# Optimization experiments

Hardware: AMD Instinct MI355X
Metric: run time of the kernel (lower is better)

Reference implementation:

```python
import jax, jax.numpy as jnp
import numpy as np
import math

B, H, S, D = 2, 8, 1024, 384
LAMBDA_INIT = 0.8 - 0.6 * math.exp(-0.3 * 1)  # depth = 1


def _clin(xr, xi, wr, wi, br=None, bi=None):
    # complex linear: (xr + i xi) @ (wr + i wi)^T + (br + i bi)
    o_r = jnp.einsum('bhse,de->bhsd', xr, wr) - jnp.einsum('bhse,de->bhsd', xi, wi)
    o_i = jnp.einsum('bhse,de->bhsd', xr, wi) + jnp.einsum('bhse,de->bhsd', xi, wr)
    if br is not None:
        o_r = o_r + br
        o_i = o_i + bi
    return o_r, o_i


def _attn_w(qr, qi, kr, ki, scale):
    # complex score magnitude -> softmax
    s_r = jnp.einsum('bhqd,bhkd->bhqk', qr, kr) + jnp.einsum('bhqd,bhkd->bhqk', qi, ki)
    s_i = jnp.einsum('bhqd,bhkd->bhqk', qi, kr) - jnp.einsum('bhqd,bhkd->bhqk', qr, ki)
    return jax.nn.softmax(jnp.sqrt(s_r ** 2 + s_i ** 2 + 1e-8) * scale, axis=-1)


def setup_inputs() -> dict:
    key = jax.random.key(0)
    ks = jax.random.split(key, 32)
    n = lambda k, sh, std=1.0: jax.random.normal(k, sh, dtype=jnp.float32) * std
    sd = 1.0 / math.sqrt(D)
    inp = {
        'q_r': n(ks[0], (B, H, S, D)), 'q_i': n(ks[1], (B, H, S, D)),
        'k_r': n(ks[2], (B, H, S, D)), 'k_i': n(ks[3], (B, H, S, D)),
        'v_r': n(ks[4], (B, H, S, D)), 'v_i': n(ks[5], (B, H, S, D)),
        'pe_q_r': n(ks[6], (B, H, S, D)), 'pe_q_i': n(ks[7], (B, H, S, D)),
        'pe_k_r': n(ks[8], (B, H, S, D)), 'pe_k_i': n(ks[9], (B, H, S, D)),
        'wq_r': n(ks[10], (2 * D, D), sd), 'wq_i': n(ks[11], (2 * D, D), sd),
        'bq_r': jnp.zeros((2 * D,), jnp.float32), 'bq_i': jnp.zeros((2 * D,), jnp.float32),
        'wk_r': n(ks[12], (D, D), sd), 'wk_i': n(ks[13], (D, D), sd),
        'bk_r': jnp.zeros((D,), jnp.float32), 'bk_i': jnp.zeros((D,), jnp.float32),
        'wv_r': n(ks[14], (D, D), sd), 'wv_i': n(ks[15], (D, D), sd),
        'bv_r': jnp.zeros((D,), jnp.float32), 'bv_i': jnp.zeros((D,), jnp.float32),
        'wg_r': n(ks[16], (D, D), sd), 'wg_i': n(ks[17], (D, D), sd),
        'bg_r': jnp.zeros((D,), jnp.float32), 'bg_i': jnp.zeros((D,), jnp.float32),
        'wo_r': n(ks[18], (D, D), sd), 'wo_i': n(ks[19], (D, D), sd),
        'bo_r': jnp.zeros((D,), jnp.float32), 'bo_i': jnp.zeros((D,), jnp.float32),
        'lam_q1': n(ks[20], (D,), 0.1), 'lam_k1': n(ks[21], (D,), 0.1),
        'lam_q2': n(ks[22], (D,), 0.1), 'lam_k2': n(ks[23], (D,), 0.1),
        'subln_w': jnp.ones((2 * D,), jnp.float32),
    }
    return inp


def reference(q_r, q_i, k_r, k_i, v_r, v_i, pe_q_r, pe_q_i, pe_k_r, pe_k_i,
              wq_r, wq_i, bq_r, bq_i, wk_r, wk_i, bk_r, bk_i,
              wv_r, wv_i, bv_r, bv_i, wg_r, wg_i, bg_r, bg_i,
              wo_r, wo_i, bo_r, bo_i, lam_q1, lam_k1, lam_q2, lam_k2, subln_w):
    scale = D ** (-0.5)
    qp_r, qp_i = _clin(q_r, q_i, wq_r, wq_i, bq_r, bq_i)   # [B,H,S,2D]
    kp_r, kp_i = _clin(k_r, k_i, wk_r, wk_i, bk_r, bk_i)   # [B,H,S,D]
    vp_r, vp_i = _clin(v_r, v_i, wv_r, wv_i, bv_r, bv_i)
    qp_r = qp_r + jnp.concatenate([pe_q_r, pe_q_r], axis=-1)
    qp_i = qp_i + jnp.concatenate([pe_q_i, pe_q_i], axis=-1)
    kp_r = kp_r + pe_k_r
    kp_i = kp_i + pe_k_i
    q1_r, q2_r = jnp.split(qp_r, 2, axis=-1)
    q1_i, q2_i = jnp.split(qp_i, 2, axis=-1)
    w1 = _attn_w(q1_r, q1_i, kp_r, kp_i, scale)
    w2 = _attn_w(q2_r, q2_i, kp_r, kp_i, scale)
    a1_r = jnp.einsum('bhqk,bhkd->bhqd', w1, vp_r)
    a1_i = jnp.einsum('bhqk,bhkd->bhqd', w1, vp_i)
    a2_r = jnp.einsum('bhqk,bhkd->bhqd', w2, vp_r)
    a2_i = jnp.einsum('bhqk,bhkd->bhqd', w2, vp_i)
    cat_r = jnp.concatenate([a1_r, a2_r], axis=-1)
    cat_i = jnp.concatenate([a1_i, a2_i], axis=-1)
    # complex RMSNorm (SubLN) over 2D dim
    rms = jnp.sqrt(jnp.mean(cat_r ** 2 + cat_i ** 2, axis=-1, keepdims=True) + 1e-5)
    cat_r = cat_r / rms * subln_w
    cat_i = cat_i / rms * subln_w
    a1_r, a2_r = jnp.split(cat_r, 2, axis=-1)
    a1_i, a2_i = jnp.split(cat_i, 2, axis=-1)
    lam1 = jnp.exp(jnp.sum(lam_q1 * lam_k1))
    lam2 = jnp.exp(jnp.sum(lam_q2 * lam_k2))
    lam = jax.nn.sigmoid(lam1 - lam2 + LAMBDA_INIT)
    out_r = a1_r - lam * a2_r
    out_i = a1_i - lam * a2_i
    g_r, g_i = _clin(q_r, q_i, wg_r, wg_i, bg_r, bg_i)
    out_r, out_i = g_r * out_r - g_i * out_i, g_r * out_i + g_i * out_r
    out_r, out_i = _clin(out_r, out_i, wo_r, wo_i, bo_r, bo_i)
    return (out_r, out_i)
```

## Files before the change

kernel.cpp:

```cpp
#include <hip/hip_runtime.h>
#include <cstdint>


typedef _Float16 f16;
typedef __attribute__((ext_vector_type(8))) _Float16 f16x8;
typedef __attribute__((ext_vector_type(4))) _Float16 f16x4;
typedef __attribute__((ext_vector_type(4))) float    f32x4;

#define NROW      16384L
#define HALF_OUT  6291456L
#define SCALE_QK  0.05103103630798288f
#define LAMBDA_INIT 0.35550906759096926f

__device__ __forceinline__ void gl2lds16(const void* g, void* l) {
  __builtin_amdgcn_global_load_lds(
      (const __attribute__((address_space(1))) void*)(uintptr_t)g,
      (__attribute__((address_space(3))) void*)(uint32_t)(uintptr_t)l,
      16, 0, 0);
}

struct PeTab { const float* p[6]; float sgn[6]; };

enum { MODE_PROJ = 0, MODE_VT = 1, MODE_OUT = 2 };

template <int MODE>
__launch_bounds__(256, 2)
__global__ void gemm_kernel(const f16* __restrict__ A, int lda,
                            const f16* __restrict__ W, int ldw,
                            const float* __restrict__ bias, PeTab pe,
                            void* __restrict__ outp, int ldo, int K, int gx)
{
  __shared__ f16 As[2][128 * 32];
  __shared__ f16 Bs[2][128 * 32];
  const int t    = threadIdx.x;
  const int lane = t & 63;
  const int wave = t >> 6;
  const int bid  = blockIdx.x;
  const int xcd  = bid & 7;
  const int per  = bid >> 3;
  const long row0 = (long)(xcd * 16 + per / gx) * 128;
  const long col0 = (long)(per % gx) * 128;
  const f16* Ab = A + row0 * (long)lda;
  const f16* Wb = W + col0 * (long)ldw;

  const int wm = (wave >> 1) * 64;
  const int wn = (wave & 1) * 64;
  const int lm = lane & 15;
  const int lk = (lane >> 4) * 8;

  f32x4 acc[4][4] = {};

  auto stage = [&](int kk, int sub) {
#pragma unroll
    for (int j = 0; j < 2; ++j) {
      int sg = j * 256 + t, r = sg >> 2, c = (sg & 3) << 3;
      gl2lds16(Ab + (long)r * lda + kk + c, &As[sub][sg * 8]);
      gl2lds16(Wb + (long)r * ldw + kk + c, &Bs[sub][sg * 8]);
    }
  };

  for (int kk = 0; kk < K; kk += 64) {
    stage(kk, 0);
    stage(kk + 32, 1);
    __syncthreads();
#pragma unroll
    for (int sub = 0; sub < 2; ++sub) {
      f16x8 bfr[4];
#pragma unroll
      for (int nt = 0; nt < 4; ++nt)
        bfr[nt] = *(const f16x8*)&Bs[sub][(wn + nt * 16 + lm) * 32 + lk];
#pragma unroll
      for (int mt = 0; mt < 4; ++mt) {
        f16x8 afr = *(const f16x8*)&As[sub][(wm + mt * 16 + lm) * 32 + lk];
#pragma unroll
        for (int nt = 0; nt < 4; ++nt)
          acc[mt][nt] = __builtin_amdgcn_mfma_f32_16x16x32_f16(afr, bfr[nt], acc[mt][nt], 0, 0, 0);
      }
    }
    __syncthreads();
  }

  const int lm4 = (lane >> 4) * 4;
  const int ln  = lane & 15;
#pragma unroll
  for (int mt = 0; mt < 4; ++mt) {
#pragma unroll
    for (int nt = 0; nt < 4; ++nt) {
      int col = (int)col0 + wn + nt * 16 + ln;
      if (MODE == MODE_VT) {
        long rowb = row0 + wm + mt * 16 + lm4;
        long bh = rowb >> 10, sx = rowb & 1023;
        f16x4 v;
#pragma unroll
        for (int r = 0; r < 4; ++r) v[r] = (f16)(acc[mt][nt][r] + bias[col]);
        *(f16x4*)&((f16*)outp)[(bh * 768 + col) * 1024 + sx] = v;
      } else {
#pragma unroll
        for (int r = 0; r < 4; ++r) {
          long row = row0 + wm + mt * 16 + lm4 + r;
          float c = acc[mt][nt][r] + bias[col];
          if (MODE == MODE_PROJ) {
            int s2 = col / 384;
            int d  = col - s2 * 384;
            const float* pp = pe.p[s2];
            if (pp) c += pe.sgn[s2] * pp[row * 384 + d];
            ((f16*)outp)[row * (long)ldo + col] = (f16)c;
          } else {
            float* of = (float*)outp;
            if (col < 384) of[row * 384 + col] = c;
            else           of[HALF_OUT + row * 384 + (col - 384)] = c;
          }
        }
      }
    }
  }
}

__launch_bounds__(256, 2)
__global__ void score_kernel(const f16* __restrict__ QG, const f16* __restrict__ Kc,
                             f16* __restrict__ P)
{
  __shared__ f16 AsL[128 * 32], AsH[128 * 32], BsL[128 * 32], BsH[128 * 32];
  const int t = threadIdx.x, lane = t & 63, wave = t >> 6;
  const int bid = blockIdx.x;
  const int xcd = bid & 7, per = bid >> 3;
  const int z   = xcd * 4 + per / 64;
  const int rem = per % 64;
  const int w = z >> 4, bh = z & 15;
  const long row0 = (long)(rem / 8) * 128, col0 = (long)(rem % 8) * 128;
  const f16* A = QG + (long)bh * 1024 * 2304 + row0 * 2304 + w * 768;
  const f16* B = Kc + (long)bh * 1024 * 768 + col0 * 768;
  f16* Pz = P + (long)z * 1024 * 1024;

  const int wm = (wave >> 1) * 64, wn = (wave & 1) * 64;
  const int lm = lane & 15, lk = (lane >> 4) * 8;
  f32x4 accr[4][4] = {}, acci[4][4] = {};

  for (int kk = 0; kk < 384; kk += 32) {
#pragma unroll
    for (int j = 0; j < 2; ++j) {
      int sg = j * 256 + t, r = sg >> 2, c = (sg & 3) << 3;
      gl2lds16(A + (long)r * 2304 + kk + c,       &AsL[sg * 8]);
      gl2lds16(A + (long)r * 2304 + 384 + kk + c, &AsH[sg * 8]);
      gl2lds16(B + (long)r * 768 + kk + c,        &BsL[sg * 8]);
      gl2lds16(B + (long)r * 768 + 384 + kk + c,  &BsH[sg * 8]);
    }
    __syncthreads();
    f16x8 bl[4], bh2[4];
#pragma unroll
    for (int nt = 0; nt < 4; ++nt) {
      bl[nt]  = *(const f16x8*)&BsL[(wn + nt * 16 + lm) * 32 + lk];
      bh2[nt] = *(const f16x8*)&BsH[(wn + nt * 16 + lm) * 32 + lk];
    }
#pragma unroll
    for (int mt = 0; mt < 4; ++mt) {
      f16x8 al  = *(const f16x8*)&AsL[(wm + mt * 16 + lm) * 32 + lk];
      f16x8 ah  = *(const f16x8*)&AsH[(wm + mt * 16 + lm) * 32 + lk];
      f16x8 nal = -al;
#pragma unroll
      for (int nt = 0; nt < 4; ++nt) {
        accr[mt][nt] = __builtin_amdgcn_mfma_f32_16x16x32_f16(al,  bl[nt],  accr[mt][nt], 0, 0, 0);
        accr[mt][nt] = __builtin_amdgcn_mfma_f32_16x16x32_f16(ah,  bh2[nt], accr[mt][nt], 0, 0, 0);
        acci[mt][nt] = __builtin_amdgcn_mfma_f32_16x16x32_f16(ah,  bl[nt],  acci[mt][nt], 0, 0, 0);
        acci[mt][nt] = __builtin_amdgcn_mfma_f32_16x16x32_f16(nal, bh2[nt], acci[mt][nt], 0, 0, 0);
      }
    }
    __syncthreads();
  }
  const int lm4 = (lane >> 4) * 4, ln = lane & 15;
#pragma unroll
  for (int mt = 0; mt < 4; ++mt)
#pragma unroll
    for (int nt = 0; nt < 4; ++nt) {
      int col = (int)col0 + wn + nt * 16 + ln;
#pragma unroll
      for (int r = 0; r < 4; ++r) {
        long row = row0 + wm + mt * 16 + lm4 + r;
        float sr = accr[mt][nt][r], si = acci[mt][nt][r];
        float m = sqrtf(sr * sr + si * si + 1e-8f) * SCALE_QK;
        Pz[row * 1024 + col] = (f16)m;
      }
    }
}

__launch_bounds__(256, 2)
__global__ void pv_kernel(const f16* __restrict__ P, const f16* __restrict__ Vt,
                          f16* __restrict__ O1, f16* __restrict__ O2)
{
  __shared__ f16 As1[2][128 * 32], As2[2][128 * 32], Bs[2][128 * 32];
  const int t = threadIdx.x, lane = t & 63, wave = t >> 6;
  const int bid = blockIdx.x;
  const int xcd = bid & 7, per = bid >> 3;
  const int bh  = xcd * 2 + per / 48;
  const int rem = per % 48;
  const long row0 = (long)(rem / 6) * 128, col0 = (long)(rem % 6) * 128;
  const f16* A1 = P + ((long)bh << 20) + row0 * 1024;
  const f16* A2 = P + ((long)(16 + bh) << 20) + row0 * 1024;
  const f16* B  = Vt + (long)bh * 768 * 1024 + col0 * 1024;

  const int wm = (wave >> 1) * 64, wn = (wave & 1) * 64;
  const int lm = lane & 15, lk = (lane >> 4) * 8;
  f32x4 ac1[4][4] = {}, ac2[4][4] = {};

  auto stage = [&](int kk, int sub) {
#pragma unroll
    for (int j = 0; j < 2; ++j) {
      int sg = j * 256 + t, r = sg >> 2, c = (sg & 3) << 3;
      gl2lds16(A1 + (long)r * 1024 + kk + c, &As1[sub][sg * 8]);
      gl2lds16(A2 + (long)r * 1024 + kk + c, &As2[sub][sg * 8]);
      gl2lds16(B  + (long)r * 1024 + kk + c, &Bs[sub][sg * 8]);
    }
  };

  for (int kk = 0; kk < 1024; kk += 64) {
    stage(kk, 0);
    stage(kk + 32, 1);
    __syncthreads();
#pragma unroll
    for (int sub = 0; sub < 2; ++sub) {
      f16x8 bfr[4];
#pragma unroll
      for (int nt = 0; nt < 4; ++nt)
        bfr[nt] = *(const f16x8*)&Bs[sub][(wn + nt * 16 + lm) * 32 + lk];
#pragma unroll
      for (int mt = 0; mt < 4; ++mt) {
        f16x8 a1 = *(const f16x8*)&As1[sub][(wm + mt * 16 + lm) * 32 + lk];
        f16x8 a2 = *(const f16x8*)&As2[sub][(wm + mt * 16 + lm) * 32 + lk];
#pragma unroll
        for (int nt = 0; nt < 4; ++nt) {
          ac1[mt][nt] = __builtin_amdgcn_mfma_f32_16x16x32_f16(a1, bfr[nt], ac1[mt][nt], 0, 0, 0);
          ac2[mt][nt] = __builtin_amdgcn_mfma_f32_16x16x32_f16(a2, bfr[nt], ac2[mt][nt], 0, 0, 0);
        }
      }
    }
    __syncthreads();
  }
  const int lm4 = (lane >> 4) * 4, ln = lane & 15;
#pragma unroll
  for (int mt = 0; mt < 4; ++mt)
#pragma unroll
    for (int nt = 0; nt < 4; ++nt) {
      int col = (int)col0 + wn + nt * 16 + ln;
#pragma unroll
      for (int r = 0; r < 4; ++r) {
        long row = (long)bh * 1024 + row0 + wm + mt * 16 + lm4 + r;
        O1[row * 768 + col] = (f16)ac1[mt][nt][r];
        O2[row * 768 + col] = (f16)ac2[mt][nt][r];
      }
    }
}

__global__ void softmax_kernel(f16* __restrict__ P)
{
  const long row = blockIdx.x;
  f16* p = P + row * 1024;
  const int lane = threadIdx.x;
  f16x8 v0 = *(const f16x8*)(p + lane * 16);
  f16x8 v1 = *(const f16x8*)(p + lane * 16 + 8);
  float x[16];
#pragma unroll
  for (int i = 0; i < 8; ++i) { x[i] = (float)v0[i]; x[8 + i] = (float)v1[i]; }
  float m = x[0];
#pragma unroll
  for (int i = 1; i < 16; ++i) m = fmaxf(m, x[i]);
#pragma unroll
  for (int off = 1; off < 64; off <<= 1) m = fmaxf(m, __shfl_xor(m, off));
  float s = 0.f;
#pragma unroll
  for (int i = 0; i < 16; ++i) { x[i] = __expf(x[i] - m); s += x[i]; }
#pragma unroll
  for (int off = 1; off < 64; off <<= 1) s += __shfl_xor(s, off);
  float inv = 1.f / s;
  f16x8 o0, o1;
#pragma unroll
  for (int i = 0; i < 8; ++i) { o0[i] = (f16)(x[i] * inv); o1[i] = (f16)(x[8 + i] * inv); }
  *(f16x8*)(p + lane * 16)     = o0;
  *(f16x8*)(p + lane * 16 + 8) = o1;
}

__global__ void fuse_kernel(const f16* __restrict__ A1, const f16* __restrict__ A2,
                            const f16* __restrict__ QG, const float* __restrict__ subw,
                            const float* __restrict__ lamp, f16* __restrict__ Xatt)
{
  const long row = blockIdx.x;
  const int t = threadIdx.x, lane = t & 63, wv = t >> 6;
  const f16* a1 = A1 + row * 768;
  const f16* a2 = A2 + row * 768;
  const f16* g  = QG + row * 2304 + 1536;
  float a1r[3], a1i[3], a2r[3], a2i[3];
  float ss = 0.f;
#pragma unroll
  for (int q = 0; q < 3; ++q) {
    int d = t + q * 128;
    a1r[q] = (float)a1[d]; a1i[q] = (float)a1[d + 384];
    a2r[q] = (float)a2[d]; a2i[q] = (float)a2[d + 384];
    ss += a1r[q] * a1r[q] + a1i[q] * a1i[q] + a2r[q] * a2r[q] + a2i[q] * a2i[q];
  }
#pragma unroll
  for (int m = 1; m < 64; m <<= 1) ss += __shfl_xor(ss, m);
  __shared__ float part[2];
  if (lane == 0) part[wv] = ss;
  __syncthreads();
  float inv = rsqrtf((part[0] + part[1]) * (1.f / 768.f) + 1e-5f);
  float lam = lamp[0];
#pragma unroll
  for (int q = 0; q < 3; ++q) {
    int d = t + q * 128;
    float w1 = subw[d], w2 = subw[d + 384];
    float n1r = a1r[q] * inv * w1, n1i = a1i[q] * inv * w1;
    float n2r = a2r[q] * inv * w2, n2i = a2i[q] * inv * w2;
    float orr = n1r - lam * n2r, oii = n1i - lam * n2i;
    float gr = (float)g[d], gi = (float)g[d + 384];
    Xatt[row * 768 + d]       = (f16)(gr * orr - gi * oii);
    Xatt[row * 768 + d + 384] = (f16)(gr * oii + gi * orr);
  }
}

__global__ void lam_kernel(const float* lq1, const float* lk1,
                           const float* lq2, const float* lk2, float* out)
{
  const int t = threadIdx.x, lane = t & 63, wv = t >> 6;
  float s1 = 0.f, s2 = 0.f;
#pragma unroll
  for (int q = 0; q < 3; ++q) {
    int d = t + q * 128;
    s1 += lq1[d] * lk1[d];
    s2 += lq2[d] * lk2[d];
  }
#pragma unroll
  for (int m = 1; m < 64; m <<= 1) { s1 += __shfl_xor(s1, m); s2 += __shfl_xor(s2, m); }
  __shared__ float p1[2], p2[2];
  if (lane == 0) { p1[wv] = s1; p2[wv] = s2; }
  __syncthreads();
  if (t == 0) {
    float x = expf(p1[0] + p1[1]) - expf(p2[0] + p2[1]) + LAMBDA_INIT;
    out[0] = 1.f / (1.f + expf(-x));
  }
}

__global__ void pack_x(const float* __restrict__ xr, const float* __restrict__ xi,
                       f16* __restrict__ X)
{
  long i = (long)blockIdx.x * 256 + threadIdx.x;
  long row = i / 768;
  int  c   = (int)(i - row * 768);
  float v = (c < 384) ? xr[row * 384 + c] : xi[row * 384 + (c - 384)];
  X[i] = (f16)v;
}

__global__ void pack_wq(const float* wq_r, const float* wq_i,
                        const float* wg_r, const float* wg_i,
                        const float* bq_r, const float* bq_i,
                        const float* bg_r, const float* bg_i,
                        f16* __restrict__ Wp, float* __restrict__ bp)
{
  long i = (long)blockIdx.x * 256 + threadIdx.x;
  int n = (int)(i / 768), e = (int)(i % 768);
  int s = n / 384, d = n - s * 384;
  int hb = (e >= 384);
  int ee = e - hb * 384;
  float v = 0.f, b = 0.f;
  switch (s) {
    case 0: v = hb ? -wq_i[d * 384 + ee]         :  wq_r[d * 384 + ee];         b = bq_r[d];       break;
    case 1: v = hb ?  wq_r[d * 384 + ee]         :  wq_i[d * 384 + ee];         b = bq_i[d];       break;
    case 2: v = hb ? -wq_i[(384 + d) * 384 + ee] :  wq_r[(384 + d) * 384 + ee]; b = bq_r[384 + d]; break;
    case 3: v = hb ?  wq_r[(384 + d) * 384 + ee] :  wq_i[(384 + d) * 384 + ee]; b = bq_i[384 + d]; break;
    case 4: v = hb ? -wg_i[d * 384 + ee]         :  wg_r[d * 384 + ee];         b = bg_r[d];       break;
    case 5: v = hb ?  wg_r[d * 384 + ee]         :  wg_i[d * 384 + ee];         b = bg_i[d];       break;
  }
  Wp[i] = (f16)v;
  if (e == 0) bp[n] = b;
}

__global__ void pack_w_std(const float* wr, const float* wi,
                           const float* br, const float* bi,
                           f16* __restrict__ Wp, float* __restrict__ bp)
{
  long i = (long)blockIdx.x * 256 + threadIdx.x;
  int n = (int)(i / 768), e = (int)(i % 768);
  int hb = (e >= 384);
  int ee = e - hb * 384;
  float v, b;
  if (n < 384) { v = hb ? -wi[n * 384 + ee] : wr[n * 384 + ee]; b = br[n]; }
  else { int d = n - 384; v = hb ? wr[d * 384 + ee] : wi[d * 384 + ee]; b = bi[d]; }
  Wp[i] = (f16)v;
  if (e == 0) bp[n] = b;
}

extern "C" void kernel_launch(void* const* d_in, const int* in_sizes, int n_in,
                              void* d_out, int out_size, void* d_ws, size_t ws_size,
                              hipStream_t stream)
{
  const float* q_r    = (const float*)d_in[0];
  const float* q_i    = (const float*)d_in[1];
  const float* k_r    = (const float*)d_in[2];
  const float* k_i    = (const float*)d_in[3];
  const float* v_r    = (const float*)d_in[4];
  const float* v_i    = (const float*)d_in[5];
  const float* pe_q_r = (const float*)d_in[6];
  const float* pe_q_i = (const float*)d_in[7];
  const float* pe_k_r = (const float*)d_in[8];
  const float* pe_k_i = (const float*)d_in[9];
  const float* wq_r = (const float*)d_in[10];
  const float* wq_i = (const float*)d_in[11];
  const float* bq_r = (const float*)d_in[12];
  const float* bq_i = (const float*)d_in[13];
  const float* wk_r = (const float*)d_in[14];
  const float* wk_i = (const float*)d_in[15];
  const float* bk_r = (const float*)d_in[16];
  const float* bk_i = (const float*)d_in[17];
  const float* wv_r = (const float*)d_in[18];
  const float* wv_i = (const float*)d_in[19];
  const float* bv_r = (const float*)d_in[20];
  const float* bv_i = (const float*)d_in[21];
  const float* wg_r = (const float*)d_in[22];
  const float* wg_i = (const float*)d_in[23];
  const float* bg_r = (const float*)d_in[24];
  const float* bg_i = (const float*)d_in[25];
  const float* wo_r = (const float*)d_in[26];
  const float* wo_i = (const float*)d_in[27];
  const float* bo_r = (const float*)d_in[28];
  const float* bo_i = (const float*)d_in[29];
  const float* lam_q1 = (const float*)d_in[30];
  const float* lam_k1 = (const float*)d_in[31];
  const float* lam_q2 = (const float*)d_in[32];
  const float* lam_k2 = (const float*)d_in[33];
  const float* subln_w = (const float*)d_in[34];

  char* base = (char*)d_ws;
  size_t off = 0;
  auto alloc = [&](size_t bytes) -> void* {
    void* p = base + off;
    off = (off + bytes + 255) & ~(size_t)255;
    return p;
  };
  f16*   Wq   = (f16*)alloc(2304L * 768 * 2);
  f16*   Wk   = (f16*)alloc(768L * 768 * 2);
  f16*   Wv   = (f16*)alloc(768L * 768 * 2);
  f16*   Wo   = (f16*)alloc(768L * 768 * 2);
  float* bq   = (float*)alloc(2304 * 4);
  float* bk   = (float*)alloc(768 * 4);
  float* bv   = (float*)alloc(768 * 4);
  float* bo   = (float*)alloc(768 * 4);
  float* lamp = (float*)alloc(4);
  f16*   X    = (f16*)alloc(NROW * 768 * 2);
  f16*   QG   = (f16*)alloc(NROW * 2304 * 2);
  f16*   Kc   = (f16*)alloc(NROW * 768 * 2);
  f16*   Vt   = (f16*)alloc(16L * 768 * 1024 * 2);
  f16*   P    = (f16*)alloc(32L * 1024 * 1024 * 2);
  if (off > ws_size) return;
  f16* A1   = Kc;
  f16* A2   = X;
  f16* Xatt = Vt;

  pack_wq<<<6912, 256, 0, stream>>>(wq_r, wq_i, wg_r, wg_i, bq_r, bq_i, bg_r, bg_i, Wq, bq);
  pack_w_std<<<2304, 256, 0, stream>>>(wk_r, wk_i, bk_r, bk_i, Wk, bk);
  pack_w_std<<<2304, 256, 0, stream>>>(wv_r, wv_i, bv_r, bv_i, Wv, bv);
  pack_w_std<<<2304, 256, 0, stream>>>(wo_r, wo_i, bo_r, bo_i, Wo, bo);
  lam_kernel<<<1, 128, 0, stream>>>(lam_q1, lam_k1, lam_q2, lam_k2, lamp);

  PeTab pe0{};

  pack_x<<<49152, 256, 0, stream>>>(q_r, q_i, X);
  PeTab peQ{};
  peQ.p[0] = pe_q_r; peQ.sgn[0] = 1.f;
  peQ.p[1] = pe_q_i; peQ.sgn[1] = 1.f;
  peQ.p[2] = pe_q_r; peQ.sgn[2] = 1.f;
  peQ.p[3] = pe_q_i; peQ.sgn[3] = 1.f;
  gemm_kernel<MODE_PROJ><<<2304, 256, 0, stream>>>(
      X, 768, Wq, 768, bq, peQ, QG, 2304, 768, 18);

  pack_x<<<49152, 256, 0, stream>>>(k_r, k_i, X);
  PeTab peK{};
  peK.p[0] = pe_k_r; peK.sgn[0] = 1.f;
  peK.p[1] = pe_k_i; peK.sgn[1] = 1.f;
  gemm_kernel<MODE_PROJ><<<768, 256, 0, stream>>>(
      X, 768, Wk, 768, bk, peK, Kc, 768, 768, 6);

  pack_x<<<49152, 256, 0, stream>>>(v_r, v_i, X);
  gemm_kernel<MODE_VT><<<768, 256, 0, stream>>>(
      X, 768, Wv, 768, bv, pe0, Vt, 0, 768, 6);

  score_kernel<<<2048, 256, 0, stream>>>(QG, Kc, P);
  softmax_kernel<<<32768, 64, 0, stream>>>(P);
  pv_kernel<<<768, 256, 0, stream>>>(P, Vt, A1, A2);

  fuse_kernel<<<16384, 128, 0, stream>>>(A1, A2, QG, subln_w, lamp, Xatt);

  gemm_kernel<MODE_OUT><<<768, 256, 0, stream>>>(
      Xatt, 768, Wo, 768, bo, pe0, d_out, 0, 768, 6);

  (void)in_sizes; (void)n_in; (void)out_size;
}
```

Before: 829.8 us.

## Double-buffer LDS staging in GEMMs and vectorize pack/softmax launches

The gemm, score and pv kernels now prefetch the next 32-wide K slice into an alternate LDS buffer while the current slice feeds the MFMAs. This is meant to hide global-load latency behind compute. The score kernel's LDS doubles to 64 KB, which may limit occupancy at two blocks per CU. pack_x now converts 8 elements per thread with a vector store, and softmax packs 4 rows per 256-thread block to cut launch and block overhead. There is only one barrier per iteration, placed after compute. That looks safe because the next prefetch goes to the buffer just read, which is fenced by that barrier, but it relies on the asynchronous LDS loads completing before the barrier.

```diff
diff --git a/kernel.cpp b/kernel.cpp
--- a/kernel.cpp
+++ b/kernel.cpp
@@ -59,25 +59,24 @@
     }
   };
 
-  for (int kk = 0; kk < K; kk += 64) {
-    stage(kk, 0);
-    stage(kk + 32, 1);
+  stage(0, 0);
+  __syncthreads();
+  int cur = 0;
+  for (int kk = 0; kk < K; kk += 32) {
+    if (kk + 32 < K) stage(kk + 32, cur ^ 1);
+    f16x8 bfr[4];
+#pragma unroll
+    for (int nt = 0; nt < 4; ++nt)
+      bfr[nt] = *(const f16x8*)&Bs[cur][(wn + nt * 16 + lm) * 32 + lk];
+#pragma unroll
+    for (int mt = 0; mt < 4; ++mt) {
+      f16x8 afr = *(const f16x8*)&As[cur][(wm + mt * 16 + lm) * 32 + lk];
+#pragma unroll
+      for (int nt = 0; nt < 4; ++nt)
+        acc[mt][nt] = __builtin_amdgcn_mfma_f32_16x16x32_f16(afr, bfr[nt], acc[mt][nt], 0, 0, 0);
+    }
     __syncthreads();
-#pragma unroll
-    for (int sub = 0; sub < 2; ++sub) {
-      f16x8 bfr[4];
-#pragma unroll
-      for (int nt = 0; nt < 4; ++nt)
-        bfr[nt] = *(const f16x8*)&Bs[sub][(wn + nt * 16 + lm) * 32 + lk];
-#pragma unroll
-      for (int mt = 0; mt < 4; ++mt) {
-        f16x8 afr = *(const f16x8*)&As[sub][(wm + mt * 16 + lm) * 32 + lk];
-#pragma unroll
-        for (int nt = 0; nt < 4; ++nt)
-          acc[mt][nt] = __builtin_amdgcn_mfma_f32_16x16x32_f16(afr, bfr[nt], acc[mt][nt], 0, 0, 0);
-      }
-    }
-    __syncthreads();
+    cur ^= 1;
   }
 
   const int lm4 = (lane >> 4) * 4;
@@ -120,7 +119,8 @@
 __global__ void score_kernel(const f16* __restrict__ QG, const f16* __restrict__ Kc,
                              f16* __restrict__ P)
 {
-  __shared__ f16 AsL[128 * 32], AsH[128 * 32], BsL[128 * 32], BsH[128 * 32];
+  __shared__ f16 AsL[2][128 * 32], AsH[2][128 * 32];
+  __shared__ f16 BsL[2][128 * 32], BsH[2][128 * 32];
   const int t = threadIdx.x, lane = t & 63, wave = t >> 6;
   const int bid = blockIdx.x;
   const int xcd = bid & 7, per = bid >> 3;
@@ -136,26 +136,32 @@
   const int lm = lane & 15, lk = (lane >> 4) * 8;
   f32x4 accr[4][4] = {}, acci[4][4] = {};
 
-  for (int kk = 0; kk < 384; kk += 32) {
+  auto stage = [&](int kk, int sub) {
 #pragma unroll
     for (int j = 0; j < 2; ++j) {
       int sg = j * 256 + t, r = sg >> 2, c = (sg & 3) << 3;
-      gl2lds16(A + (long)r * 2304 + kk + c,       &AsL[sg * 8]);
-      gl2lds16(A + (long)r * 2304 + 384 + kk + c, &AsH[sg * 8]);
-      gl2lds16(B + (long)r * 768 + kk + c,        &BsL[sg * 8]);
-      gl2lds16(B + (long)r * 768 + 384 + kk + c,  &BsH[sg * 8]);
-    }
-    __syncthreads();
+      gl2lds16(A + (long)r * 2304 + kk + c,       &AsL[sub][sg * 8]);
+      gl2lds16(A + (long)r * 2304 + 384 + kk + c, &AsH[sub][sg * 8]);
+      gl2lds16(B + (long)r * 768 + kk + c,        &BsL[sub][sg * 8]);
+      gl2lds16(B + (long)r * 768 + 384 + kk + c,  &BsH[sub][sg * 8]);
+    }
+  };
+
+  stage(0, 0);
+  __syncthreads();
+  int cur = 0;
+  for (int kk = 0; kk < 384; kk += 32) {
+    if (kk + 32 < 384) stage(kk + 32, cur ^ 1);
     f16x8 bl[4], bh2[4];
 #pragma unroll
     for (int nt = 0; nt < 4; ++nt) {
-      bl[nt]  = *(const f16x8*)&BsL[(wn + nt * 16 + lm) * 32 + lk];
-      bh2[nt] = *(const f16x8*)&BsH[(wn + nt * 16 + lm) * 32 + lk];
+      bl[nt]  = *(const f16x8*)&BsL[cur][(wn + nt * 16 + lm) * 32 + lk];
+      bh2[nt] = *(const f16x8*)&BsH[cur][(wn + nt * 16 + lm) * 32 + lk];
     }
 #pragma unroll
     for (int mt = 0; mt < 4; ++mt) {
-      f16x8 al  = *(const f16x8*)&AsL[(wm + mt * 16 + lm) * 32 + lk];
-      f16x8 ah  = *(const f16x8*)&AsH[(wm + mt * 16 + lm) * 32 + lk];
+      f16x8 al  = *(const f16x8*)&AsL[cur][(wm + mt * 16 + lm) * 32 + lk];
+      f16x8 ah  = *(const f16x8*)&AsH[cur][(wm + mt * 16 + lm) * 32 + lk];
       f16x8 nal = -al;
 #pragma unroll
       for (int nt = 0; nt < 4; ++nt) {
@@ -166,6 +172,7 @@
       }
     }
     __syncthreads();
+    cur ^= 1;
   }
   const int lm4 = (lane >> 4) * 4, ln = lane & 15;
 #pragma unroll
@@ -212,28 +219,27 @@
     }
   };
 
-  for (int kk = 0; kk < 1024; kk += 64) {
-    stage(kk, 0);
-    stage(kk + 32, 1);
+  stage(0, 0);
+  __syncthreads();
+  int cur = 0;
+  for (int kk = 0; kk < 1024; kk += 32) {
+    if (kk + 32 < 1024) stage(kk + 32, cur ^ 1);
+    f16x8 bfr[4];
+#pragma unroll
+    for (int nt = 0; nt < 4; ++nt)
+      bfr[nt] = *(const f16x8*)&Bs[cur][(wn + nt * 16 + lm) * 32 + lk];
+#pragma unroll
+    for (int mt = 0; mt < 4; ++mt) {
+      f16x8 a1 = *(const f16x8*)&As1[cur][(wm + mt * 16 + lm) * 32 + lk];
+      f16x8 a2 = *(const f16x8*)&As2[cur][(wm + mt * 16 + lm) * 32 + lk];
+#pragma unroll
+      for (int nt = 0; nt < 4; ++nt) {
+        ac1[mt][nt] = __builtin_amdgcn_mfma_f32_16x16x32_f16(a1, bfr[nt], ac1[mt][nt], 0, 0, 0);
+        ac2[mt][nt] = __builtin_amdgcn_mfma_f32_16x16x32_f16(a2, bfr[nt], ac2[mt][nt], 0, 0, 0);
+      }
+    }
     __syncthreads();
-#pragma unroll
-    for (int sub = 0; sub < 2; ++sub) {
-      f16x8 bfr[4];
-#pragma unroll
-      for (int nt = 0; nt < 4; ++nt)
-        bfr[nt] = *(const f16x8*)&Bs[sub][(wn + nt * 16 + lm) * 32 + lk];
-#pragma unroll
-      for (int mt = 0; mt < 4; ++mt) {
-        f16x8 a1 = *(const f16x8*)&As1[sub][(wm + mt * 16 + lm) * 32 + lk];
-        f16x8 a2 = *(const f16x8*)&As2[sub][(wm + mt * 16 + lm) * 32 + lk];
-#pragma unroll
-        for (int nt = 0; nt < 4; ++nt) {
-          ac1[mt][nt] = __builtin_amdgcn_mfma_f32_16x16x32_f16(a1, bfr[nt], ac1[mt][nt], 0, 0, 0);
-          ac2[mt][nt] = __builtin_amdgcn_mfma_f32_16x16x32_f16(a2, bfr[nt], ac2[mt][nt], 0, 0, 0);
-        }
-      }
-    }
-    __syncthreads();
+    cur ^= 1;
   }
   const int lm4 = (lane >> 4) * 4, ln = lane & 15;
 #pragma unroll
@@ -252,9 +258,9 @@
 
 __global__ void softmax_kernel(f16* __restrict__ P)
 {
-  const long row = blockIdx.x;
+  const long row = (long)blockIdx.x * 4 + (threadIdx.x >> 6);
   f16* p = P + row * 1024;
-  const int lane = threadIdx.x;
+  const int lane = threadIdx.x & 63;
   f16x8 v0 = *(const f16x8*)(p + lane * 16);
   f16x8 v1 = *(const f16x8*)(p + lane * 16 + 8);
   float x[16];
@@ -342,10 +348,14 @@
                        f16* __restrict__ X)
 {
   long i = (long)blockIdx.x * 256 + threadIdx.x;
-  long row = i / 768;
-  int  c   = (int)(i - row * 768);
-  float v = (c < 384) ? xr[row * 384 + c] : xi[row * 384 + (c - 384)];
-  X[i] = (f16)v;
+  long row = i / 96;
+  int  rem = (int)(i - row * 96);
+  int  c   = rem * 8;
+  const float* src = (c < 384) ? (xr + row * 384 + c) : (xi + row * 384 + (c - 384));
+  f16x8 o;
+#pragma unroll
+  for (int j = 0; j < 8; ++j) o[j] = (f16)src[j];
+  *(f16x8*)&X[row * 768 + c] = o;
 }
 
 __global__ void pack_wq(const float* wq_r, const float* wq_i,
@@ -461,7 +471,7 @@
 
   PeTab pe0{};
 
-  pack_x<<<49152, 256, 0, stream>>>(q_r, q_i, X);
+  pack_x<<<6144, 256, 0, stream>>>(q_r, q_i, X);
   PeTab peQ{};
   peQ.p[0] = pe_q_r; peQ.sgn[0] = 1.f;
   peQ.p[1] = pe_q_i; peQ.sgn[1] = 1.f;
@@ -470,19 +480,19 @@
   gemm_kernel<MODE_PROJ><<<2304, 256, 0, stream>>>(
       X, 768, Wq, 768, bq, peQ, QG, 2304, 768, 18);
 
-  pack_x<<<49152, 256, 0, stream>>>(k_r, k_i, X);
+  pack_x<<<6144, 256, 0, stream>>>(k_r, k_i, X);
   PeTab peK{};
   peK.p[0] = pe_k_r; peK.sgn[0] = 1.f;
   peK.p[1] = pe_k_i; peK.sgn[1] = 1.f;
   gemm_kernel<MODE_PROJ><<<768, 256, 0, stream>>>(
       X, 768, Wk, 768, bk, peK, Kc, 768, 768, 6);
 
-  pack_x<<<49152, 256, 0, stream>>>(v_r, v_i, X);
+  pack_x<<<6144, 256, 0, stream>>>(v_r, v_i, X);
   gemm_kernel<MODE_VT><<<768, 256, 0, stream>>>(
       X, 768, Wv, 768, bv, pe0, Vt, 0, 768, 6);
 
   score_kernel<<<2048, 256, 0, stream>>>(QG, Kc, P);
-  softmax_kernel<<<32768, 64, 0, stream>>>(P);
+  softmax_kernel<<<8192, 256, 0, stream>>>(P);
   pv_kernel<<<768, 256, 0, stream>>>(P, Vt, A1, A2);
 
   fuse_kernel<<<16384, 128, 0, stream>>>(A1, A2, QG, subln_w, lamp, Xatt);
```

Result: faster. 787.3 us (-5.1%).
